# Performance work log

Hardware: AMD Instinct MI355X
Metric: run time of the kernel (lower is better)

Reference implementation:

```python
import jax, jax.numpy as jnp
import numpy as np

NEG_INF = -1.0e9  # matches torch masked_fill value

def setup_inputs() -> dict:
    key = jax.random.key(0)
    kq, kk, kv, km = jax.random.split(key, 4)
    B, S, D = 16, 2048, 128
    query = jax.random.normal(kq, (B, S, D), dtype=jnp.float32)
    k = jax.random.normal(kk, (B, S, D), dtype=jnp.float32)
    value = jax.random.normal(kv, (B, S, D), dtype=jnp.float32)
    mask = jax.random.randint(km, (B, S, S), 0, 2).astype(jnp.bool_)
    return {"query": query, "key": k, "value": value, "mask": mask}

def reference(query, key, value, mask):
    # scores: [B, Sq, Sk]
    D = key.shape[-1]
    scale = jnp.sqrt(jnp.asarray(D, dtype=query.dtype))
    scores = jnp.einsum('bqd,bkd->bqk', query, key) / scale
    scores = jnp.where(mask, jnp.asarray(NEG_INF, dtype=scores.dtype), scores)
    attn = jax.nn.softmax(scores, axis=2)
    # dropout p=0.0 -> identity in eval/reference
    out = jnp.einsum('bqk,bkd->bqd', attn, value)
    return out, attn
```

## Files before the change

kernel.cpp:

```cpp
#include <hip/hip_runtime.h>

#define S 2048
#define Dh 128
#define NB 16
#define OUT_ELEMS ((size_t)NB * S * Dh)
#define NEG_BIG -1.0e9f
#define SCALE 0.08838834764831845f

typedef __attribute__((ext_vector_type(8))) short bf16x8;
typedef __attribute__((ext_vector_type(4))) float f32x4;
typedef __attribute__((ext_vector_type(4))) short s16x4;

__device__ __forceinline__ short f2bf(float x) {
    unsigned u = __float_as_uint(x);
    u += 0x7fffu + ((u >> 16) & 1u);
    return (short)(u >> 16);
}

__device__ __forceinline__ s16x4 pack4(float4 v) {
    s16x4 r;
    r.x = f2bf(v.x); r.y = f2bf(v.y); r.z = f2bf(v.z); r.w = f2bf(v.w);
    return r;
}

__global__ void detect_mask(const unsigned char* __restrict__ m, int* __restrict__ flag) {
    __shared__ int any;
    if (threadIdx.x == 0) any = 0;
    __syncthreads();
    int t = threadIdx.x;
    unsigned char v = (unsigned char)(m[t * 4 + 1] | m[t * 4 + 2] | m[t * 4 + 3]);
    if (v) atomicOr(&any, 1);
    __syncthreads();
    if (t == 0) *flag = any;
}

__global__ __launch_bounds__(256) void transpose_v(const float* __restrict__ V,
                                                   short* __restrict__ Vt) {
    const int kb = blockIdx.x, b = blockIdx.y;
    const float* Vb = V + ((size_t)b * S + kb * 64) * Dh;
    short* VtB = Vt + (size_t)b * Dh * S;
    __shared__ float Ls[64][132];
    const int t = threadIdx.x;
#pragma unroll
    for (int i = 0; i < 8; i++) {
        int idx = t + i * 256;
        int r = idx >> 5, c = (idx & 31) << 2;
        *(float4*)&Ls[r][c] = *(const float4*)(Vb + r * Dh + c);
    }
    __syncthreads();
#pragma unroll
    for (int i = 0; i < 8; i++) {
        int idx = t + i * 256;
        int n = idx >> 4, kc = (idx & 15) << 2;
        s16x4 o;
        o.x = f2bf(Ls[kc + 0][n]);
        o.y = f2bf(Ls[kc + 1][n]);
        o.z = f2bf(Ls[kc + 2][n]);
        o.w = f2bf(Ls[kc + 3][n]);
        *(s16x4*)(VtB + (size_t)n * S + kb * 64 + kc) = o;
    }
}

__global__ __launch_bounds__(256, 2) void qk_kernel(const float* __restrict__ Q,
                                                    const float* __restrict__ Km,
                                                    float* __restrict__ Sc,
                                                    const void* __restrict__ maskp,
                                                    const int* __restrict__ flagp,
                                                    float2* __restrict__ part,
                                                    const int fuse) {
    const int kt = blockIdx.x, qt = blockIdx.y, b = blockIdx.z;
    const float* Qb = Q + ((size_t)b * S + qt * 128) * Dh;
    const float* Kb = Km + ((size_t)b * S + kt * 128) * Dh;
    __shared__ short As[128][72];
    __shared__ short Bs[128][72];
    __shared__ __align__(16) unsigned char Ms[128][144];
    const int t = threadIdx.x;
    const int w = t >> 6, lane = t & 63, fr = lane & 15, quad = lane >> 4;
    const int mw = (w >> 1) * 64, nw = (w & 1) * 64;
    f32x4 acc[4][4] = {};

    if (fuse) {
        const int flag = *flagp;
        if (flag) {
            const unsigned char* Mb = (const unsigned char*)maskp + ((size_t)b * S + qt * 128) * S + (size_t)kt * 128;
#pragma unroll
            for (int i = 0; i < 4; i++) {
                int idx = t + i * 256;
                int r = idx >> 3, c = (idx & 7) * 16;
                *(int4*)&Ms[r][c] = *(const int4*)(Mb + (size_t)r * S + c);
            }
        } else {
            const int* Mb = (const int*)maskp + ((size_t)b * S + qt * 128) * S + (size_t)kt * 128;
#pragma unroll
            for (int i = 0; i < 16; i++) {
                int idx = t + i * 256;
                int r = idx >> 5, c = (idx & 31) * 4;
                int4 m = *(const int4*)(Mb + (size_t)r * S + c);
                uchar4 o;
                o.x = (unsigned char)(m.x != 0);
                o.y = (unsigned char)(m.y != 0);
                o.z = (unsigned char)(m.z != 0);
                o.w = (unsigned char)(m.w != 0);
                *(uchar4*)&Ms[r][c] = o;
            }
        }
    }

    for (int k0 = 0; k0 < Dh; k0 += 64) {
        __syncthreads();
#pragma unroll
        for (int i = 0; i < 8; i++) {
            int idx = t + i * 256;
            int r = idx >> 4, c = (idx & 15) << 2;
            float4 qv = *(const float4*)(Qb + r * Dh + k0 + c);
            float4 kv = *(const float4*)(Kb + r * Dh + k0 + c);
            *(s16x4*)&As[r][c] = pack4(qv);
            *(s16x4*)&Bs[r][c] = pack4(kv);
        }
        __syncthreads();
#pragma unroll
        for (int kc = 0; kc < 2; kc++) {
            const int ko = kc * 32 + quad * 8;
            bf16x8 af[4], bf[4];
#pragma unroll
            for (int mi = 0; mi < 4; mi++) af[mi] = *(const bf16x8*)&As[mw + mi * 16 + fr][ko];
#pragma unroll
            for (int ni = 0; ni < 4; ni++) bf[ni] = *(const bf16x8*)&Bs[nw + ni * 16 + fr][ko];
#pragma unroll
            for (int mi = 0; mi < 4; mi++)
#pragma unroll
                for (int ni = 0; ni < 4; ni++)
                    acc[mi][ni] = __builtin_amdgcn_mfma_f32_16x16x32_bf16(af[mi], bf[ni], acc[mi][ni], 0, 0, 0);
        }
    }

    __syncthreads();
    float2* pm = (float2*)&As[0][0];
    float* ScB = Sc + (size_t)b * S * S;
#pragma unroll
    for (int mi = 0; mi < 4; mi++)
#pragma unroll
        for (int r = 0; r < 4; r++) {
            const int lrow = mw + mi * 16 + quad * 4 + r;
            const size_t grow = (size_t)(qt * 128 + lrow);
            float s[4];
#pragma unroll
            for (int ni = 0; ni < 4; ni++) {
                const int lcol = nw + ni * 16 + fr;
                float v = acc[mi][ni][r] * SCALE;
                if (fuse && Ms[lrow][lcol]) v = NEG_BIG;
                s[ni] = v;
                ScB[grow * S + kt * 128 + lcol] = v;
            }
            if (fuse) {
                float mx = fmaxf(fmaxf(s[0], s[1]), fmaxf(s[2], s[3]));
#pragma unroll
                for (int o = 8; o > 0; o >>= 1) mx = fmaxf(mx, __shfl_xor(mx, o, 64));
                float l = __expf(s[0] - mx) + __expf(s[1] - mx) +
                          __expf(s[2] - mx) + __expf(s[3] - mx);
#pragma unroll
                for (int o = 8; o > 0; o >>= 1) l += __shfl_xor(l, o, 64);
                if (fr == 0) pm[lrow * 2 + (w & 1)] = make_float2(mx, l);
            }
        }

    if (fuse) {
        __syncthreads();
        if (t < 128) {
            float2 a = pm[t * 2 + 0], c = pm[t * 2 + 1];
            float M = fmaxf(a.x, c.x);
            float L = a.y * __expf(a.x - M) + c.y * __expf(c.x - M);
            part[((size_t)(b * 16 + kt)) * S + qt * 128 + t] = make_float2(M, L);
        }
    }
}

__global__ __launch_bounds__(256) void reduce_stats(const float2* __restrict__ part,
                                                    float2* __restrict__ stats) {
    const int rid = blockIdx.x * 256 + threadIdx.x;
    const int b = rid >> 11, row = rid & (S - 1);
    float2 p[16];
    float M = -3.4e38f;
#pragma unroll
    for (int kt = 0; kt < 16; kt++) {
        p[kt] = part[((size_t)(b * 16 + kt)) * S + row];
        M = fmaxf(M, p[kt].x);
    }
    float L = 0.f;
#pragma unroll
    for (int kt = 0; kt < 16; kt++) L += p[kt].y * __expf(p[kt].x - M);
    stats[rid] = make_float2(M, 1.0f / L);
}

__global__ __launch_bounds__(256) void softmax_kernel(float* __restrict__ Sc,
                                                      const void* __restrict__ maskp,
                                                      const int* __restrict__ flagp) {
    const int b = blockIdx.y;
    const int w = threadIdx.x >> 6, lane = threadIdx.x & 63;
    const int row = blockIdx.x * 4 + w;
    float* R = Sc + ((size_t)b * S + row) * S;
    float4* R4 = (float4*)R;
    const int flag = flagp ? *flagp : 0;

    float sv[32];
    if (flag) {
        const uchar4* M4 = (const uchar4*)((const unsigned char*)maskp + ((size_t)b * S + row) * S);
#pragma unroll
        for (int j = 0; j < 8; j++) {
            float4 v = R4[lane + 64 * j];
            uchar4 m = M4[lane + 64 * j];
            sv[4 * j + 0] = m.x ? NEG_BIG : v.x;
            sv[4 * j + 1] = m.y ? NEG_BIG : v.y;
            sv[4 * j + 2] = m.z ? NEG_BIG : v.z;
            sv[4 * j + 3] = m.w ? NEG_BIG : v.w;
        }
    } else {
        const int4* M4 = (const int4*)((const int*)maskp + ((size_t)b * S + row) * S);
#pragma unroll
        for (int j = 0; j < 8; j++) {
            float4 v = R4[lane + 64 * j];
            int4 m = M4[lane + 64 * j];
            sv[4 * j + 0] = m.x ? NEG_BIG : v.x;
            sv[4 * j + 1] = m.y ? NEG_BIG : v.y;
            sv[4 * j + 2] = m.z ? NEG_BIG : v.z;
            sv[4 * j + 3] = m.w ? NEG_BIG : v.w;
        }
    }

    float mx = sv[0];
#pragma unroll
    for (int i = 1; i < 32; i++) mx = fmaxf(mx, sv[i]);
    for (int o = 32; o > 0; o >>= 1) mx = fmaxf(mx, __shfl_xor(mx, o, 64));

    float sum = 0.f;
#pragma unroll
    for (int i = 0; i < 32; i++) {
        sv[i] = __expf(sv[i] - mx);
        sum += sv[i];
    }
    for (int o = 32; o > 0; o >>= 1) sum += __shfl_xor(sum, o, 64);
    const float inv = 1.0f / sum;

#pragma unroll
    for (int j = 0; j < 8; j++) {
        float4 p;
        p.x = sv[4 * j + 0] * inv;
        p.y = sv[4 * j + 1] * inv;
        p.z = sv[4 * j + 2] * inv;
        p.w = sv[4 * j + 3] * inv;
        R4[lane + 64 * j] = p;
    }
}

__global__ __launch_bounds__(256, 2) void pv_kernel(float* __restrict__ Sc,
                                                    const float* __restrict__ V,
                                                    const short* __restrict__ Vt,
                                                    const int useVt,
                                                    float* __restrict__ Out,
                                                    const float2* __restrict__ stats,
                                                    const int fuse) {
    const int mt = blockIdx.x, b = blockIdx.y;
    float* ScB = Sc + (size_t)b * S * S + (size_t)mt * 64 * S;
    const float* Vb = V + (size_t)b * S * Dh;
    const short* VtB = Vt + (size_t)b * Dh * S;
    float* OutB = Out + ((size_t)b * S + mt * 64) * Dh;
    __shared__ short As[64][72];
    __shared__ float2 sstat[64];
    const int t = threadIdx.x, w = t >> 6, lane = t & 63, fr = lane & 15, quad = lane >> 4;
    const int mw = (w >> 1) * 32, nw = (w & 1) * 64;
    f32x4 acc[2][4] = {};

    if (fuse && t < 64) sstat[t] = stats[(size_t)b * S + mt * 64 + t];

    for (int k0 = 0; k0 < S; k0 += 64) {
        __syncthreads();
#pragma unroll
        for (int i = 0; i < 4; i++) {
            int idx = t + i * 256;
            int r = idx >> 4, c = (idx & 15) << 2;
            float4 v = *(const float4*)(ScB + (size_t)r * S + k0 + c);
            if (fuse) {
                float2 st = sstat[r];
                v.x = __expf(v.x - st.x) * st.y;
                v.y = __expf(v.y - st.x) * st.y;
                v.z = __expf(v.z - st.x) * st.y;
                v.w = __expf(v.w - st.x) * st.y;
                *(float4*)(ScB + (size_t)r * S + k0 + c) = v;
            }
            *(s16x4*)&As[r][c] = pack4(v);
        }
        __syncthreads();
#pragma unroll
        for (int kc = 0; kc < 2; kc++) {
            const int ko = kc * 32 + quad * 8;
            bf16x8 af[2], bf[4];
#pragma unroll
            for (int mi = 0; mi < 2; mi++) af[mi] = *(const bf16x8*)&As[mw + mi * 16 + fr][ko];
            if (useVt) {
#pragma unroll
                for (int ni = 0; ni < 4; ni++)
                    bf[ni] = *(const bf16x8*)(VtB + (size_t)(nw + ni * 16 + fr) * S + k0 + ko);
            } else {
#pragma unroll
                for (int ni = 0; ni < 4; ni++) {
                    int n = nw + ni * 16 + fr;
#pragma unroll
                    for (int j = 0; j < 8; j++) bf[ni][j] = f2bf(Vb[(size_t)(k0 + ko + j) * Dh + n]);
                }
            }
#pragma unroll
            for (int mi = 0; mi < 2; mi++)
#pragma unroll
                for (int ni = 0; ni < 4; ni++)
                    acc[mi][ni] = __builtin_amdgcn_mfma_f32_16x16x32_bf16(af[mi], bf[ni], acc[mi][ni], 0, 0, 0);
        }
    }

#pragma unroll
    for (int mi = 0; mi < 2; mi++)
#pragma unroll
        for (int ni = 0; ni < 4; ni++)
#pragma unroll
            for (int r = 0; r < 4; r++) {
                int row = mw + mi * 16 + quad * 4 + r;
                int col = nw + ni * 16 + fr;
                OutB[(size_t)row * Dh + col] = acc[mi][ni][r];
            }
}

extern "C" void kernel_launch(void* const* d_in, const int* in_sizes, int n_in,
                              void* d_out, int out_size, void* d_ws, size_t ws_size,
                              hipStream_t stream) {
    const float* Q = (const float*)d_in[0];
    const float* Km = (const float*)d_in[1];
    const float* V = (const float*)d_in[2];
    const void* M = d_in[3];
    float* out = (float*)d_out;
    float* attn = out + OUT_ELEMS;

    const size_t VT_BYTES = (size_t)NB * Dh * S * sizeof(short);
    const size_t STATS_BYTES = (size_t)NB * S * sizeof(float2);

    int useVt = 0, fuse = 0;
    short* Vt = nullptr;
    float2* stats = nullptr;
    int* flag = nullptr;

    if (ws_size >= VT_BYTES + STATS_BYTES + 64) {
        useVt = 1; fuse = 1;
        Vt = (short*)d_ws;
        stats = (float2*)((char*)d_ws + VT_BYTES);
        flag = (int*)((char*)d_ws + VT_BYTES + STATS_BYTES);
    } else if (ws_size >= VT_BYTES + 64) {
        useVt = 1;
        Vt = (short*)d_ws;
        flag = (int*)((char*)d_ws + VT_BYTES);
    } else if (ws_size >= 64) {
        flag = (int*)d_ws;
    }

    float2* part = (float2*)d_out;

    if (flag) detect_mask<<<1, 256, 0, stream>>>((const unsigned char*)M, flag);
    if (useVt) transpose_v<<<dim3(32, NB), 256, 0, stream>>>(V, Vt);

    qk_kernel<<<dim3(16, 16, NB), 256, 0, stream>>>(Q, Km, attn, M, flag, part, fuse);

    if (fuse) {
        reduce_stats<<<dim3((NB * S) / 256), 256, 0, stream>>>(part, stats);
        pv_kernel<<<dim3(32, NB), 256, 0, stream>>>(attn, V, Vt, useVt, out, stats, 1);
    } else {
        softmax_kernel<<<dim3(512, NB), 256, 0, stream>>>(attn, M, flag);
        pv_kernel<<<dim3(32, NB), 256, 0, stream>>>(attn, V, Vt, useVt, out, nullptr, 0);
    }
}
```

Baseline: 762.9 us.

## Recompute QK in fused PV kernel to avoid round-tripping raw scores through HBM

Adds a new path: Q and K are pre-converted to bf16, a stats-only QK kernel computes per-row max and sum without writing scores, and a fused kernel recomputes QK^T, applies mask and softmax normalization, writes attn once, and multiplies by V. This removes the write-then-read-then-rewrite of the large score matrix that the old path performed, at the cost of computing QK twice and needing more workspace. The new path runs only if the workspace is large enough; otherwise the old path is used.

```diff
diff --git a/kernel.cpp b/kernel.cpp
--- a/kernel.cpp
+++ b/kernel.cpp
@@ -59,6 +59,314 @@
         o.w = f2bf(Ls[kc + 3][n]);
         *(s16x4*)(VtB + (size_t)n * S + kb * 64 + kc) = o;
     }
+}
+
+__global__ __launch_bounds__(256) void cvt_bf16(const float* __restrict__ in,
+                                                short* __restrict__ out) {
+    const size_t n4 = (size_t)NB * S * Dh / 4;
+    for (size_t i = (size_t)blockIdx.x * 256 + threadIdx.x; i < n4; i += (size_t)gridDim.x * 256) {
+        float4 v = ((const float4*)in)[i];
+        ((s16x4*)out)[i] = pack4(v);
+    }
+}
+
+__global__ __launch_bounds__(256, 2) void qk_stats(const short* __restrict__ Qbf,
+                                                   const short* __restrict__ Kbf,
+                                                   const void* __restrict__ maskp,
+                                                   const int* __restrict__ flagp,
+                                                   float2* __restrict__ part) {
+    const int kt = blockIdx.x, qt = blockIdx.y, b = blockIdx.z;
+    const short* Qb = Qbf + ((size_t)b * S + qt * 128) * Dh;
+    const short* Kb = Kbf + ((size_t)b * S + kt * 128) * Dh;
+    __shared__ short As[128][72];
+    __shared__ short Bs[128][72];
+    __shared__ __align__(16) unsigned char Ms[128][144];
+    const int t = threadIdx.x;
+    const int w = t >> 6, lane = t & 63, fr = lane & 15, quad = lane >> 4;
+    const int mw = (w >> 1) * 64, nw = (w & 1) * 64;
+    f32x4 acc[4][4] = {};
+
+    const int flag = *flagp;
+    if (flag) {
+        const unsigned char* Mb = (const unsigned char*)maskp + ((size_t)b * S + qt * 128) * S + (size_t)kt * 128;
+#pragma unroll
+        for (int i = 0; i < 4; i++) {
+            int idx = t + i * 256;
+            int r = idx >> 3, c = (idx & 7) * 16;
+            *(int4*)&Ms[r][c] = *(const int4*)(Mb + (size_t)r * S + c);
+        }
+    } else {
+        const int* Mb = (const int*)maskp + ((size_t)b * S + qt * 128) * S + (size_t)kt * 128;
+#pragma unroll
+        for (int i = 0; i < 16; i++) {
+            int idx = t + i * 256;
+            int r = idx >> 5, c = (idx & 31) * 4;
+            int4 m = *(const int4*)(Mb + (size_t)r * S + c);
+            uchar4 o;
+            o.x = (unsigned char)(m.x != 0);
+            o.y = (unsigned char)(m.y != 0);
+            o.z = (unsigned char)(m.z != 0);
+            o.w = (unsigned char)(m.w != 0);
+            *(uchar4*)&Ms[r][c] = o;
+        }
+    }
+
+    for (int k0 = 0; k0 < Dh; k0 += 64) {
+        __syncthreads();
+#pragma unroll
+        for (int i = 0; i < 4; i++) {
+            int idx = t + i * 256;
+            int r = idx >> 3, c8 = (idx & 7) * 8;
+            *(bf16x8*)&As[r][c8] = *(const bf16x8*)(Qb + (size_t)r * Dh + k0 + c8);
+            *(bf16x8*)&Bs[r][c8] = *(const bf16x8*)(Kb + (size_t)r * Dh + k0 + c8);
+        }
+        __syncthreads();
+#pragma unroll
+        for (int kc = 0; kc < 2; kc++) {
+            const int ko = kc * 32 + quad * 8;
+            bf16x8 af[4], bf[4];
+#pragma unroll
+            for (int mi = 0; mi < 4; mi++) af[mi] = *(const bf16x8*)&As[mw + mi * 16 + fr][ko];
+#pragma unroll
+            for (int ni = 0; ni < 4; ni++) bf[ni] = *(const bf16x8*)&Bs[nw + ni * 16 + fr][ko];
+#pragma unroll
+            for (int mi = 0; mi < 4; mi++)
+#pragma unroll
+                for (int ni = 0; ni < 4; ni++)
+                    acc[mi][ni] = __builtin_amdgcn_mfma_f32_16x16x32_bf16(af[mi], bf[ni], acc[mi][ni], 0, 0, 0);
+        }
+    }
+
+    __syncthreads();
+    float2* pm = (float2*)&As[0][0];
+#pragma unroll
+    for (int mi = 0; mi < 4; mi++)
+#pragma unroll
+        for (int r = 0; r < 4; r++) {
+            const int lrow = mw + mi * 16 + quad * 4 + r;
+            float s[4];
+#pragma unroll
+            for (int ni = 0; ni < 4; ni++) {
+                const int lcol = nw + ni * 16 + fr;
+                float v = acc[mi][ni][r] * SCALE;
+                if (Ms[lrow][lcol]) v = NEG_BIG;
+                s[ni] = v;
+            }
+            float mx = fmaxf(fmaxf(s[0], s[1]), fmaxf(s[2], s[3]));
+#pragma unroll
+            for (int o = 8; o > 0; o >>= 1) mx = fmaxf(mx, __shfl_xor(mx, o, 64));
+            float l = __expf(s[0] - mx) + __expf(s[1] - mx) +
+                      __expf(s[2] - mx) + __expf(s[3] - mx);
+#pragma unroll
+            for (int o = 8; o > 0; o >>= 1) l += __shfl_xor(l, o, 64);
+            if (fr == 0) pm[lrow * 2 + (w & 1)] = make_float2(mx, l);
+        }
+
+    __syncthreads();
+    if (t < 128) {
+        float2 a = pm[t * 2 + 0], c = pm[t * 2 + 1];
+        float M = fmaxf(a.x, c.x);
+        float L = a.y * __expf(a.x - M) + c.y * __expf(c.x - M);
+        part[((size_t)(b * 16 + kt)) * S + qt * 128 + t] = make_float2(M, L);
+    }
+}
+
+__global__ __launch_bounds__(256) void reduce_stats(const float2* __restrict__ part,
+                                                    float2* __restrict__ stats) {
+    const int rid = blockIdx.x * 256 + threadIdx.x;
+    const int b = rid >> 11, row = rid & (S - 1);
+    float2 p[16];
+    float M = -3.4e38f;
+#pragma unroll
+    for (int kt = 0; kt < 16; kt++) {
+        p[kt] = part[((size_t)(b * 16 + kt)) * S + row];
+        M = fmaxf(M, p[kt].x);
+    }
+    float L = 0.f;
+#pragma unroll
+    for (int kt = 0; kt < 16; kt++) L += p[kt].y * __expf(p[kt].x - M);
+    stats[rid] = make_float2(M, 1.0f / L);
+}
+
+__global__ __launch_bounds__(256, 2) void fused_pv(const short* __restrict__ Qbf,
+                                                   const short* __restrict__ Kbf,
+                                                   const short* __restrict__ Vt,
+                                                   const void* __restrict__ maskp,
+                                                   const int* __restrict__ flagp,
+                                                   const float2* __restrict__ stats,
+                                                   float* __restrict__ Attn,
+                                                   float* __restrict__ Out) {
+    const int qt = blockIdx.x, b = blockIdx.y;
+    const short* QbfB = Qbf + ((size_t)b * S + qt * 64) * Dh;
+    const short* KbfB = Kbf + (size_t)b * S * Dh;
+    const short* VtB  = Vt  + (size_t)b * Dh * S;
+    float* AttnB = Attn + ((size_t)b * S + qt * 64) * S;
+    float* OutB  = Out  + ((size_t)b * S + qt * 64) * Dh;
+    const int flag = *flagp;
+
+    __shared__ short Qs[2][64][72];
+    __shared__ short Ks[2][128][72];
+    __shared__ short Ps[2][64][72];
+    unsigned char (*Ms)[128] = (unsigned char (*)[128]) &Ps[0][0][0];
+
+    const int t = threadIdx.x, w = t >> 6, lane = t & 63, fr = lane & 15, quad = lane >> 4;
+    const int mo = (w >> 1) * 32, no = (w & 1) * 64;
+
+#pragma unroll
+    for (int i = 0; i < 4; i++) {
+        int idx = t + i * 256;
+        int r = idx >> 4, c8 = (idx & 15) * 8;
+        *(bf16x8*)&Qs[c8 >> 6][r][c8 & 63] = *(const bf16x8*)(QbfB + (size_t)r * Dh + c8);
+    }
+
+    float2 st[2][4];
+#pragma unroll
+    for (int mi = 0; mi < 2; mi++)
+#pragma unroll
+        for (int r = 0; r < 4; r++)
+            st[mi][r] = stats[(size_t)b * S + qt * 64 + mo + mi * 16 + quad * 4 + r];
+
+    f32x4 acc_o[2][4] = {};
+
+    bf16x8 kv[8];
+    int4 mreg[2];
+#pragma unroll
+    for (int i = 0; i < 8; i++) {
+        int idx = t + i * 256;
+        int r = idx >> 4, c8 = (idx & 15) * 8;
+        kv[i] = *(const bf16x8*)(KbfB + (size_t)r * Dh + c8);
+    }
+    if (flag) {
+        const unsigned char* Mb = (const unsigned char*)maskp + ((size_t)b * S + qt * 64) * S;
+#pragma unroll
+        for (int i = 0; i < 2; i++) {
+            int idx = t + i * 256;
+            int r = idx >> 3, c16 = (idx & 7) * 16;
+            mreg[i] = *(const int4*)(Mb + (size_t)r * S + c16);
+        }
+    }
+
+    for (int kt = 0; kt < 16; kt++) {
+        __syncthreads();
+#pragma unroll
+        for (int i = 0; i < 8; i++) {
+            int idx = t + i * 256;
+            int r = idx >> 4, c8 = (idx & 15) * 8;
+            *(bf16x8*)&Ks[c8 >> 6][r][c8 & 63] = kv[i];
+        }
+        if (flag) {
+#pragma unroll
+            for (int i = 0; i < 2; i++) {
+                int idx = t + i * 256;
+                int r = idx >> 3, c16 = (idx & 7) * 16;
+                *(int4*)&Ms[r][c16] = mreg[i];
+            }
+        } else {
+            const int* Mb = (const int*)maskp + ((size_t)b * S + qt * 64) * S + (size_t)kt * 128;
+#pragma unroll
+            for (int i = 0; i < 8; i++) {
+                int idx = t + i * 256;
+                int r = idx >> 5, c4 = (idx & 31) * 4;
+                int4 m = *(const int4*)(Mb + (size_t)r * S + c4);
+                uchar4 o;
+                o.x = (unsigned char)(m.x != 0);
+                o.y = (unsigned char)(m.y != 0);
+                o.z = (unsigned char)(m.z != 0);
+                o.w = (unsigned char)(m.w != 0);
+                *(uchar4*)&Ms[r][c4] = o;
+            }
+        }
+        __syncthreads();
+
+        if (kt < 15) {
+#pragma unroll
+            for (int i = 0; i < 8; i++) {
+                int idx = t + i * 256;
+                int r = idx >> 4, c8 = (idx & 15) * 8;
+                kv[i] = *(const bf16x8*)(KbfB + (size_t)((kt + 1) * 128 + r) * Dh + c8);
+            }
+            if (flag) {
+                const unsigned char* Mb = (const unsigned char*)maskp + ((size_t)b * S + qt * 64) * S + (size_t)(kt + 1) * 128;
+#pragma unroll
+                for (int i = 0; i < 2; i++) {
+                    int idx = t + i * 256;
+                    int r = idx >> 3, c16 = (idx & 7) * 16;
+                    mreg[i] = *(const int4*)(Mb + (size_t)r * S + c16);
+                }
+            }
+        }
+
+        f32x4 acc_s[2][4] = {};
+#pragma unroll
+        for (int ks = 0; ks < 4; ks++) {
+            const int h = ks >> 1, o = (ks & 1) * 32 + quad * 8;
+            bf16x8 af[2], bf[4];
+#pragma unroll
+            for (int mi = 0; mi < 2; mi++) af[mi] = *(const bf16x8*)&Qs[h][mo + mi * 16 + fr][o];
+#pragma unroll
+            for (int ni = 0; ni < 4; ni++) bf[ni] = *(const bf16x8*)&Ks[h][no + ni * 16 + fr][o];
+#pragma unroll
+            for (int mi = 0; mi < 2; mi++)
+#pragma unroll
+                for (int ni = 0; ni < 4; ni++)
+                    acc_s[mi][ni] = __builtin_amdgcn_mfma_f32_16x16x32_bf16(af[mi], bf[ni], acc_s[mi][ni], 0, 0, 0);
+        }
+
+        short ps[2][4][4];
+#pragma unroll
+        for (int mi = 0; mi < 2; mi++)
+#pragma unroll
+            for (int ni = 0; ni < 4; ni++)
+#pragma unroll
+                for (int r = 0; r < 4; r++) {
+                    const int row = mo + mi * 16 + quad * 4 + r;
+                    const int col = no + ni * 16 + fr;
+                    float v = acc_s[mi][ni][r] * SCALE;
+                    if (Ms[row][col]) v = NEG_BIG;
+                    float p = __expf(v - st[mi][r].x) * st[mi][r].y;
+                    AttnB[(size_t)row * S + kt * 128 + col] = p;
+                    ps[mi][ni][r] = f2bf(p);
+                }
+        __syncthreads();
+#pragma unroll
+        for (int mi = 0; mi < 2; mi++)
+#pragma unroll
+            for (int ni = 0; ni < 4; ni++)
+#pragma unroll
+                for (int r = 0; r < 4; r++) {
+                    const int row = mo + mi * 16 + quad * 4 + r;
+                    const int col = no + ni * 16 + fr;
+                    Ps[col >> 6][row][col & 63] = ps[mi][ni][r];
+                }
+        __syncthreads();
+
+#pragma unroll
+        for (int ks = 0; ks < 4; ks++) {
+            const int h = ks >> 1, o = (ks & 1) * 32 + quad * 8;
+            bf16x8 paf[2], pbf[4];
+#pragma unroll
+            for (int mi = 0; mi < 2; mi++) paf[mi] = *(const bf16x8*)&Ps[h][mo + mi * 16 + fr][o];
+#pragma unroll
+            for (int ni = 0; ni < 4; ni++)
+                pbf[ni] = *(const bf16x8*)(VtB + (size_t)(no + ni * 16 + fr) * S + kt * 128 + ks * 32 + quad * 8);
+#pragma unroll
+            for (int mi = 0; mi < 2; mi++)
+#pragma unroll
+                for (int ni = 0; ni < 4; ni++)
+                    acc_o[mi][ni] = __builtin_amdgcn_mfma_f32_16x16x32_bf16(paf[mi], pbf[ni], acc_o[mi][ni], 0, 0, 0);
+        }
+    }
+
+#pragma unroll
+    for (int mi = 0; mi < 2; mi++)
+#pragma unroll
+        for (int ni = 0; ni < 4; ni++)
+#pragma unroll
+            for (int r = 0; r < 4; r++) {
+                const int row = mo + mi * 16 + quad * 4 + r;
+                const int col = no + ni * 16 + fr;
+                OutB[(size_t)row * Dh + col] = acc_o[mi][ni][r];
+            }
 }
 
 __global__ __launch_bounds__(256, 2) void qk_kernel(const float* __restrict__ Q,
@@ -175,23 +483,6 @@
     }
 }
 
-__global__ __launch_bounds__(256) void reduce_stats(const float2* __restrict__ part,
-                                                    float2* __restrict__ stats) {
-    const int rid = blockIdx.x * 256 + threadIdx.x;
-    const int b = rid >> 11, row = rid & (S - 1);
-    float2 p[16];
-    float M = -3.4e38f;
-#pragma unroll
-    for (int kt = 0; kt < 16; kt++) {
-        p[kt] = part[((size_t)(b * 16 + kt)) * S + row];
-        M = fmaxf(M, p[kt].x);
-    }
-    float L = 0.f;
-#pragma unroll
-    for (int kt = 0; kt < 16; kt++) L += p[kt].y * __expf(p[kt].x - M);
-    stats[rid] = make_float2(M, 1.0f / L);
-}
-
 __global__ __launch_bounds__(256) void softmax_kernel(float* __restrict__ Sc,
                                                       const void* __restrict__ maskp,
                                                       const int* __restrict__ flagp) {
@@ -280,11 +571,11 @@
             int r = idx >> 4, c = (idx & 15) << 2;
             float4 v = *(const float4*)(ScB + (size_t)r * S + k0 + c);
             if (fuse) {
-                float2 st = sstat[r];
-                v.x = __expf(v.x - st.x) * st.y;
-                v.y = __expf(v.y - st.x) * st.y;
-                v.z = __expf(v.z - st.x) * st.y;
-                v.w = __expf(v.w - st.x) * st.y;
+                float2 stv = sstat[r];
+                v.x = __expf(v.x - stv.x) * stv.y;
+                v.y = __expf(v.y - stv.x) * stv.y;
+                v.z = __expf(v.z - stv.x) * stv.y;
+                v.w = __expf(v.w - stv.x) * stv.y;
                 *(float4*)(ScB + (size_t)r * S + k0 + c) = v;
             }
             *(s16x4*)&As[r][c] = pack4(v);
@@ -338,8 +629,30 @@
     float* out = (float*)d_out;
     float* attn = out + OUT_ELEMS;
 
-    const size_t VT_BYTES = (size_t)NB * Dh * S * sizeof(short);
+    const size_t VT_BYTES   = (size_t)NB * Dh * S * sizeof(short);
+    const size_t QBF_BYTES  = (size_t)NB * S * Dh * sizeof(short);
+    const size_t KBF_BYTES  = QBF_BYTES;
     const size_t STATS_BYTES = (size_t)NB * S * sizeof(float2);
+    const size_t REQ_NEW = VT_BYTES + QBF_BYTES + KBF_BYTES + STATS_BYTES + 64;
+
+    float2* part = (float2*)d_out;
+
+    if (ws_size >= REQ_NEW) {
+        short* Vt   = (short*)d_ws;
+        short* Qbf  = (short*)((char*)d_ws + VT_BYTES);
+        short* Kbf  = (short*)((char*)d_ws + VT_BYTES + QBF_BYTES);
+        float2* stats = (float2*)((char*)d_ws + VT_BYTES + QBF_BYTES + KBF_BYTES);
+        int* flag = (int*)((char*)d_ws + VT_BYTES + QBF_BYTES + KBF_BYTES + STATS_BYTES);
+
+        detect_mask<<<1, 256, 0, stream>>>((const unsigned char*)M, flag);
+        transpose_v<<<dim3(32, NB), 256, 0, stream>>>(V, Vt);
+        cvt_bf16<<<2048, 256, 0, stream>>>(Q, Qbf);
+        cvt_bf16<<<2048, 256, 0, stream>>>(Km, Kbf);
+        qk_stats<<<dim3(16, 16, NB), 256, 0, stream>>>(Qbf, Kbf, M, flag, part);
+        reduce_stats<<<dim3((NB * S) / 256), 256, 0, stream>>>(part, stats);
+        fused_pv<<<dim3(32, NB), 256, 0, stream>>>(Qbf, Kbf, Vt, M, flag, stats, attn, out);
+        return;
+    }
 
     int useVt = 0, fuse = 0;
     short* Vt = nullptr;
@@ -359,8 +672,6 @@
         flag = (int*)d_ws;
     }
 
-    float2* part = (float2*)d_out;
-
     if (flag) detect_mask<<<1, 256, 0, stream>>>((const unsigned char*)M, flag);
     if (useVt) transpose_v<<<dim3(32, NB), 256, 0, stream>>>(V, Vt);
 
```

Result: faster. 691.5 us (-9.4%).
